# Performance work log

Hardware: AMD Instinct MI355X
Metric: run time of the kernel (lower is better)

The kernel has to match this reference:

```python
import jax, jax.numpy as jnp
import numpy as np

CHUNK = 64

def _l2norm(x, eps=1e-6):
    return x / jnp.sqrt(jnp.sum(x * x, axis=-1, keepdims=True) + eps)

def setup_inputs() -> dict:
    key = jax.random.key(0)
    ks = jax.random.split(key, 5)
    B, S, H, Dk, Dv = 2, 4096, 16, 128, 128
    q = jax.random.normal(ks[0], (B, S, H, Dk), jnp.float32)
    k = jax.random.normal(ks[1], (B, S, H, Dk), jnp.float32)
    v = jax.random.normal(ks[2], (B, S, H, Dv), jnp.float32)
    g = -jax.random.uniform(ks[3], (B, S, H), jnp.float32)          # log-decay, negative
    beta = jax.random.uniform(ks[4], (B, S, H), jnp.float32)        # (0,1) learning rate
    return {"query": q, "key": k, "value": v, "g": g, "beta": beta}

def reference(query, key, value, g, beta):
    C = CHUNK
    init_dtype = query.dtype
    # [b, s, h, d] -> [b, h, s, d], fp32
    q = jnp.transpose(query, (0, 2, 1, 3)).astype(jnp.float32)
    k = jnp.transpose(key, (0, 2, 1, 3)).astype(jnp.float32)
    v = jnp.transpose(value, (0, 2, 1, 3)).astype(jnp.float32)
    gg = jnp.transpose(g, (0, 2, 1)).astype(jnp.float32)
    bb = jnp.transpose(beta, (0, 2, 1)).astype(jnp.float32)
    # use_qk_l2norm_in_kernel=True
    q = _l2norm(q)
    k = _l2norm(k)
    gg = jnp.clip(gg, -20.0, 20.0)
    B, H, S, Dk = k.shape
    Dv = v.shape[-1]
    pad = (-S) % C
    if pad:
        q = jnp.pad(q, ((0, 0), (0, 0), (0, pad), (0, 0)))
        k = jnp.pad(k, ((0, 0), (0, 0), (0, pad), (0, 0)))
        v = jnp.pad(v, ((0, 0), (0, 0), (0, pad), (0, 0)))
        gg = jnp.pad(gg, ((0, 0), (0, 0), (0, pad)))
        bb = jnp.pad(bb, ((0, 0), (0, 0), (0, pad)))
    T = S + pad
    N = T // C
    q = q * (1.0 / np.sqrt(Dk).astype(np.float32))
    v_beta = v * bb[..., None]
    k_beta = k * bb[..., None]
    # chunk: [b, h, n, c, d]
    qc = q.reshape(B, H, N, C, Dk)
    kc = k.reshape(B, H, N, C, Dk)
    vc = v.reshape(B, H, N, C, Dv)
    kbc = k_beta.reshape(B, H, N, C, Dk)
    vbc = v_beta.reshape(B, H, N, C, Dv)
    gc = jnp.cumsum(gg.reshape(B, H, N, C), axis=-1)
    tril = jnp.tril(jnp.ones((C, C), bool))
    strict = jnp.tril(jnp.ones((C, C), bool), -1)
    # decay_mask[i,j] = exp(g_i - g_j) on lower triangle (incl diag), else 0
    gd = gc[..., :, None] - gc[..., None, :]
    decay = jnp.where(tril, jnp.exp(jnp.where(tril, gd, 0.0)), 0.0)
    # UT transform: torch's in-place row loop computes Tm = (I - A)^{-1} with
    # A = -(k_beta @ k^T * decay) on the strictly lower triangle.
    kk = jnp.einsum('bhnik,bhnjk->bhnij', kbc, kc)
    A = jnp.where(strict, -(kk * decay), 0.0)
    I = jnp.eye(C, dtype=jnp.float32)
    Tm = jax.scipy.linalg.solve_triangular(I - A, jnp.broadcast_to(I, A.shape), lower=True, unit_diagonal=True)
    v_ut = jnp.einsum('bhnij,bhnjd->bhnid', Tm, vbc)
    k_cumdecay = jnp.einsum('bhnij,bhnjd->bhnid', Tm, kbc * jnp.exp(gc)[..., None])
    # sequential inter-chunk recurrence
    xs = tuple(jnp.moveaxis(a, 2, 0) for a in (qc, kc, v_ut, k_cumdecay, gc, decay))
    S0 = jnp.zeros((B, H, Dk, Dv), jnp.float32)
    def step(state, x):
        qi, ki, vi, kci, gi, dmi = x
        attn = jnp.where(tril, jnp.einsum('bhik,bhjk->bhij', qi, ki) * dmi, 0.0)
        v_prime = jnp.einsum('bhik,bhkd->bhid', kci, state)
        v_new = vi - v_prime
        inter = jnp.einsum('bhik,bhkd->bhid', qi * jnp.exp(gi)[..., None], state)
        out = inter + jnp.einsum('bhij,bhjd->bhid', attn, v_new)
        g_last = gi[..., -1]
        k_dec = ki * jnp.exp(g_last[..., None] - gi)[..., None]
        new_state = state * jnp.exp(g_last)[..., None, None] + jnp.einsum('bhik,bhid->bhkd', k_dec, v_new)
        return new_state, out
    _, outs = jax.lax.scan(step, S0, xs)  # outs: [n, b, h, c, dv]
    out = jnp.moveaxis(outs, 0, 2).reshape(B, H, T, Dv)[:, :, :S]
    return jnp.transpose(out, (0, 2, 1, 3)).astype(init_dtype)
```

## Files before the change

### kernel.cpp

```cpp
#include <hip/hip_runtime.h>
#include <math.h>


#define CC 64

constexpr int B_  = 2;
constexpr int S_  = 4096;
constexpr int H_  = 16;
constexpr int DK_ = 128;
constexpr int DV_ = 128;
constexpr int NC_  = S_ / CC;
constexpr int NCH_ = B_ * H_ * NC_;
constexpr int W_   = 16;
constexpr int NWB_ = DV_ / W_;

constexpr float QSCALE = 0.08838834764831845f;

constexpr size_t WS_KCUM = 0;
constexpr size_t WS_VUT  = WS_KCUM + (size_t)NCH_ * CC * DK_;
constexpr size_t WS_ATT  = WS_VUT  + (size_t)NCH_ * CC * DV_;
constexpr size_t WS_GC   = WS_ATT  + (size_t)NCH_ * CC * CC;
constexpr size_t WS_END  = WS_GC   + (size_t)NCH_ * CC;

__device__ __forceinline__ float dot4(const float4 a, const float4 b) {
    return a.x * b.x + a.y * b.y + a.z * b.z + a.w * b.w;
}

__global__ __launch_bounds__(256) void gdn_prep(
    const float* __restrict__ q, const float* __restrict__ k,
    const float* __restrict__ v, const float* __restrict__ g,
    const float* __restrict__ beta, float* __restrict__ ws)
{
    const int cid = blockIdx.x;
    const int n   = cid & (NC_ - 1);
    const int bh  = cid / NC_;
    const int h   = bh & (H_ - 1);
    const int b   = bh / H_;
    const int t   = threadIdx.x;
    const int s0  = n * CC;

    __shared__ float s_k[CC][132];
    __shared__ float s_q[CC][132];
    __shared__ float s_u[CC][132];
    __shared__ float s_A[CC][65];
    __shared__ float s_gc[CC];
    __shared__ float s_beta[CC];

    if (t < CC) {
        const size_t gi = ((size_t)b * S_ + s0 + t) * H_ + h;
        float gv = g[gi];
        s_gc[t]   = fminf(fmaxf(gv, -20.f), 20.f);
        s_beta[t] = beta[gi];
    }
    __syncthreads();
    if (t < CC) {
        float x = s_gc[t];
#pragma unroll
        for (int o = 1; o < CC; o <<= 1) {
            float y = __shfl_up(x, o);
            if (t >= o) x += y;
        }
        s_gc[t] = x;
    }

    {
        const int i  = t >> 2;
        const int d0 = (t & 3) * 32;
        const size_t rb = (((size_t)b * S_ + s0 + i) * H_ + h) * (size_t)DK_;
        float4 qr[8], kr[8];
        float ssq = 0.f, ssk = 0.f;
#pragma unroll
        for (int j4 = 0; j4 < 8; ++j4) {
            qr[j4] = *(const float4*)(q + rb + d0 + j4 * 4);
            kr[j4] = *(const float4*)(k + rb + d0 + j4 * 4);
            ssq += dot4(qr[j4], qr[j4]);
            ssk += dot4(kr[j4], kr[j4]);
        }
        ssq += __shfl_xor(ssq, 1); ssq += __shfl_xor(ssq, 2);
        ssk += __shfl_xor(ssk, 1); ssk += __shfl_xor(ssk, 2);
        const float rq = QSCALE / sqrtf(ssq + 1e-6f);
        const float rk = 1.0f   / sqrtf(ssk + 1e-6f);
#pragma unroll
        for (int j4 = 0; j4 < 8; ++j4) {
            *(float4*)&s_q[i][d0 + j4 * 4] =
                make_float4(qr[j4].x * rq, qr[j4].y * rq, qr[j4].z * rq, qr[j4].w * rq);
            *(float4*)&s_k[i][d0 + j4 * 4] =
                make_float4(kr[j4].x * rk, kr[j4].y * rk, kr[j4].z * rk, kr[j4].w * rk);
        }
    }
    __syncthreads();

    {
        const int ti = t >> 4, tj = t & 15;
        const int i0 = ti * 4, j0 = tj * 4;
        float dq[4][4] = {};
        float dkk[4][4] = {};
        if (j0 <= i0 + 3) {
#pragma unroll 2
            for (int d4 = 0; d4 < 32; ++d4) {
                float4 qa[4], ka[4], kb[4];
#pragma unroll
                for (int r = 0; r < 4; ++r) {
                    qa[r] = *(const float4*)&s_q[i0 + r][d4 * 4];
                    ka[r] = *(const float4*)&s_k[i0 + r][d4 * 4];
                    kb[r] = *(const float4*)&s_k[j0 + r][d4 * 4];
                }
#pragma unroll
                for (int r = 0; r < 4; ++r)
#pragma unroll
                    for (int c = 0; c < 4; ++c) {
                        dq[r][c]  += dot4(qa[r], kb[c]);
                        dkk[r][c] += dot4(ka[r], kb[c]);
                    }
            }
        }
        const size_t attb = WS_ATT + (size_t)cid * CC * CC;
#pragma unroll
        for (int r = 0; r < 4; ++r)
#pragma unroll
            for (int c = 0; c < 4; ++c) {
                const int i = i0 + r, j = j0 + c;
                float av = 0.f;
                if (j <= i) {
                    const float dec = expf(s_gc[i] - s_gc[j]);
                    av = dq[r][c] * dec;
                    if (j < i) s_A[i][j] = -(s_beta[i] * dkk[r][c]) * dec;
                }
                ws[attb + i * CC + j] = av;
            }
    }
    __syncthreads();

    {
        const int d = t & 127;
        if (t < 128) {
#pragma unroll 4
            for (int i = 0; i < CC; ++i)
                s_u[i][d] = v[(((size_t)b * S_ + s0 + i) * H_ + h) * (size_t)DV_ + d] * s_beta[i];
        } else {
#pragma unroll 4
            for (int i = 0; i < CC; ++i)
                s_q[i][d] = s_k[i][d] * (s_beta[i] * expf(s_gc[i]));
        }
        float* u = (t < 128) ? &s_u[0][0] : &s_q[0][0];
        for (int blk = 0; blk < 16; ++blk) {
            const int i0 = blk * 4;
            const float u0 = u[(i0 + 0) * 132 + d];
            const float u1 = u[(i0 + 1) * 132 + d] + s_A[i0 + 1][i0] * u0;
            const float u2 = u[(i0 + 2) * 132 + d] + s_A[i0 + 2][i0] * u0 + s_A[i0 + 2][i0 + 1] * u1;
            const float u3 = u[(i0 + 3) * 132 + d] + s_A[i0 + 3][i0] * u0 + s_A[i0 + 3][i0 + 1] * u1
                                                   + s_A[i0 + 3][i0 + 2] * u2;
            u[(i0 + 1) * 132 + d] = u1;
            u[(i0 + 2) * 132 + d] = u2;
            u[(i0 + 3) * 132 + d] = u3;
            for (int i = i0 + 4; i < CC; ++i) {
                const float* Ai = s_A[i];
                u[i * 132 + d] += Ai[i0] * u0 + Ai[i0 + 1] * u1 + Ai[i0 + 2] * u2 + Ai[i0 + 3] * u3;
            }
        }
    }
    __syncthreads();

    {
        const size_t kcb = WS_KCUM + (size_t)cid * CC * DK_;
        const size_t vub = WS_VUT  + (size_t)cid * CC * DV_;
        for (int p = t; p < CC * DK_; p += 256) {
            ws[kcb + p] = s_q[p >> 7][p & 127];
            ws[vub + p] = s_u[p >> 7][p & 127];
        }
        if (t < CC) ws[WS_GC + (size_t)cid * CC + t] = s_gc[t];
    }
}

__global__ __launch_bounds__(256) void gdn_scan(
    const float* __restrict__ q, const float* __restrict__ k,
    const float* __restrict__ ws, float* __restrict__ out)
{
    const int bh  = blockIdx.x & 31;
    const int wb  = blockIdx.x >> 5;
    const int h   = bh & (H_ - 1);
    const int b   = bh / H_;
    const int dv0 = wb * W_;
    const int t   = threadIdx.x;

    __shared__ float s_st[W_][132];
    __shared__ float s_qg[CC][132];
    __shared__ float s_kc[CC][132];
    __shared__ float s_kdT[DK_][CC + 4];
    __shared__ float s_vnT[W_][CC + 4];
    __shared__ float s_at[CC][CC + 4];
    __shared__ float s_gc[CC], s_eg[CC], s_edec[CC];
    __shared__ float s_egl;

    for (int p = t; p < W_ * 132; p += 256) (&s_st[0][0])[p] = 0.f;
    __syncthreads();

    const int dp = t & (W_ - 1);
    const int ig = t >> 4;

    for (int n = 0; n < NC_; ++n) {
        const int cid = bh * NC_ + n;
        const int s0  = n * CC;

        if (t < CC) s_gc[t] = ws[WS_GC + (size_t)cid * CC + t];
        __syncthreads();

        if (t < CC) {
            const float gl = s_gc[CC - 1];
            s_eg[t]   = expf(s_gc[t]);
            s_edec[t] = expf(gl - s_gc[t]);
            if (t == 0) s_egl = expf(gl);
        }
        {
            const size_t kcb = WS_KCUM + (size_t)cid * CC * DK_;
#pragma unroll
            for (int it = 0; it < (CC * DK_) / (256 * 4); ++it) {
                const int p4 = (it * 256 + t) * 4;
                *(float4*)&s_kc[p4 >> 7][p4 & 127] = *(const float4*)(ws + kcb + p4);
            }
            const size_t atb = WS_ATT + (size_t)cid * CC * CC;
#pragma unroll
            for (int it = 0; it < (CC * CC) / (256 * 4); ++it) {
                const int p4 = (it * 256 + t) * 4;
                *(float4*)&s_at[p4 >> 6][p4 & 63] = *(const float4*)(ws + atb + p4);
            }
        }
        __syncthreads();

        {
            const int i  = t >> 2;
            const int d0 = (t & 3) * 32;
            const size_t rb = (((size_t)b * S_ + s0 + i) * H_ + h) * (size_t)DK_;
            float4 qr[8], kr[8];
            float ssq = 0.f, ssk = 0.f;
#pragma unroll
            for (int j4 = 0; j4 < 8; ++j4) {
                qr[j4] = *(const float4*)(q + rb + d0 + j4 * 4);
                kr[j4] = *(const float4*)(k + rb + d0 + j4 * 4);
                ssq += dot4(qr[j4], qr[j4]);
                ssk += dot4(kr[j4], kr[j4]);
            }
            ssq += __shfl_xor(ssq, 1); ssq += __shfl_xor(ssq, 2);
            ssk += __shfl_xor(ssk, 1); ssk += __shfl_xor(ssk, 2);
            const float rq  = QSCALE / sqrtf(ssq + 1e-6f) * s_eg[i];
            const float rkd = s_edec[i] / sqrtf(ssk + 1e-6f);
#pragma unroll
            for (int j4 = 0; j4 < 8; ++j4) {
                *(float4*)&s_qg[i][d0 + j4 * 4] =
                    make_float4(qr[j4].x * rq, qr[j4].y * rq, qr[j4].z * rq, qr[j4].w * rq);
                const int d = d0 + j4 * 4;
                s_kdT[d + 0][i] = kr[j4].x * rkd;
                s_kdT[d + 1][i] = kr[j4].y * rkd;
                s_kdT[d + 2][i] = kr[j4].z * rkd;
                s_kdT[d + 3][i] = kr[j4].w * rkd;
            }
        }
        __syncthreads();

        {
            const size_t vub = WS_VUT + (size_t)cid * CC * DV_ + dv0 + dp;
            float acc[4];
#pragma unroll
            for (int r = 0; r < 4; ++r) acc[r] = ws[vub + (size_t)(ig * 4 + r) * DV_];
            for (int d4 = 0; d4 < 32; ++d4) {
                const float4 st = *(const float4*)&s_st[dp][d4 * 4];
#pragma unroll
                for (int r = 0; r < 4; ++r) {
                    const float4 kc = *(const float4*)&s_kc[ig * 4 + r][d4 * 4];
                    acc[r] -= dot4(kc, st);
                }
            }
#pragma unroll
            for (int r = 0; r < 4; ++r) s_vnT[dp][ig * 4 + r] = acc[r];
        }
        __syncthreads();

        {
            float acc[4] = {0.f, 0.f, 0.f, 0.f};
            for (int d4 = 0; d4 < 32; ++d4) {
                const float4 st = *(const float4*)&s_st[dp][d4 * 4];
#pragma unroll
                for (int r = 0; r < 4; ++r) {
                    const float4 qg = *(const float4*)&s_qg[ig * 4 + r][d4 * 4];
                    acc[r] += dot4(qg, st);
                }
            }
            for (int j4 = 0; j4 < 16; ++j4) {
                const float4 vn = *(const float4*)&s_vnT[dp][j4 * 4];
#pragma unroll
                for (int r = 0; r < 4; ++r) {
                    const float4 at = *(const float4*)&s_at[ig * 4 + r][j4 * 4];
                    acc[r] += dot4(at, vn);
                }
            }
#pragma unroll
            for (int r = 0; r < 4; ++r) {
                const int i = ig * 4 + r;
                out[(((size_t)b * S_ + s0 + i) * H_ + h) * (size_t)DV_ + dv0 + dp] = acc[r];
            }
        }
        __syncthreads();

        {
            const float egl = s_egl;
            float acc[8];
#pragma unroll
            for (int a = 0; a < 8; ++a) acc[a] = s_st[dp][ig + 16 * a] * egl;
            for (int j4 = 0; j4 < 16; ++j4) {
                const float4 vn = *(const float4*)&s_vnT[dp][j4 * 4];
#pragma unroll
                for (int a = 0; a < 8; ++a) {
                    const float4 kd = *(const float4*)&s_kdT[ig + 16 * a][j4 * 4];
                    acc[a] += dot4(kd, vn);
                }
            }
#pragma unroll
            for (int a = 0; a < 8; ++a) s_st[dp][ig + 16 * a] = acc[a];
        }
        __syncthreads();
    }
}

extern "C" void kernel_launch(void* const* d_in, const int* in_sizes, int n_in,
                              void* d_out, int out_size, void* d_ws, size_t ws_size,
                              hipStream_t stream) {
    const float* q    = (const float*)d_in[0];
    const float* k    = (const float*)d_in[1];
    const float* v    = (const float*)d_in[2];
    const float* g    = (const float*)d_in[3];
    const float* beta = (const float*)d_in[4];
    float* ws  = (float*)d_ws;
    float* out = (float*)d_out;

    gdn_prep<<<NCH_, 256, 0, stream>>>(q, k, v, g, beta, ws);
    gdn_scan<<<B_ * H_ * NWB_, 256, 0, stream>>>(q, k, ws, out);
}
```

Baseline: 1.353 ms.

## Rework prep and scan kernels with 512 threads and split-K register tiles

Both kernels move from 256 to 512 threads per block. The matmuls now use 4x4 register tiles with split-K across lanes and shuffle reductions. The scan kernel stores the state as [Dk][Dv] and stacks the k_cumdecay and scaled-q rows into one shared tile, so a single GEMM produces both v_prime and the inter-chunk output. It also fuses the intra-chunk output with the state update behind one barrier, cutting the barriers per chunk. The prep kernel stages the attention matrix in shared memory and writes all workspace tiles with float4 stores. The cost is higher register pressure and extra shuffle traffic.

```diff
diff --git a/kernel.cpp b/kernel.cpp
--- a/kernel.cpp
+++ b/kernel.cpp
@@ -20,13 +20,16 @@
 constexpr size_t WS_VUT  = WS_KCUM + (size_t)NCH_ * CC * DK_;
 constexpr size_t WS_ATT  = WS_VUT  + (size_t)NCH_ * CC * DV_;
 constexpr size_t WS_GC   = WS_ATT  + (size_t)NCH_ * CC * CC;
-constexpr size_t WS_END  = WS_GC   + (size_t)NCH_ * CC;
-
-__device__ __forceinline__ float dot4(const float4 a, const float4 b) {
-    return a.x * b.x + a.y * b.y + a.z * b.z + a.w * b.w;
+
+__device__ __forceinline__ void ld4(float* d, const float* s) {
+    float4 t = *(const float4*)s;
+    d[0] = t.x; d[1] = t.y; d[2] = t.z; d[3] = t.w;
 }
-
-__global__ __launch_bounds__(256) void gdn_prep(
+__device__ __forceinline__ void st4(float* d, const float* s) {
+    *(float4*)d = make_float4(s[0], s[1], s[2], s[3]);
+}
+
+__global__ __launch_bounds__(512) void gdn_prep(
     const float* __restrict__ q, const float* __restrict__ k,
     const float* __restrict__ v, const float* __restrict__ g,
     const float* __restrict__ beta, float* __restrict__ ws)
@@ -41,20 +44,16 @@
 
     __shared__ float s_k[CC][132];
     __shared__ float s_q[CC][132];
-    __shared__ float s_u[CC][132];
-    __shared__ float s_A[CC][65];
+    __shared__ float s_A[CC][66];
+    __shared__ float s_at[CC][68];
     __shared__ float s_gc[CC];
     __shared__ float s_beta[CC];
 
     if (t < CC) {
         const size_t gi = ((size_t)b * S_ + s0 + t) * H_ + h;
         float gv = g[gi];
-        s_gc[t]   = fminf(fmaxf(gv, -20.f), 20.f);
+        float x = fminf(fmaxf(gv, -20.f), 20.f);
         s_beta[t] = beta[gi];
-    }
-    __syncthreads();
-    if (t < CC) {
-        float x = s_gc[t];
 #pragma unroll
         for (int o = 1; o < CC; o <<= 1) {
             float y = __shfl_up(x, o);
@@ -64,61 +63,69 @@
     }
 
     {
-        const int i  = t >> 2;
-        const int d0 = (t & 3) * 32;
+        const int i  = t >> 3;
+        const int d0 = (t & 7) * 16;
         const size_t rb = (((size_t)b * S_ + s0 + i) * H_ + h) * (size_t)DK_;
-        float4 qr[8], kr[8];
+        float qr[4][4], kr[4][4];
         float ssq = 0.f, ssk = 0.f;
 #pragma unroll
-        for (int j4 = 0; j4 < 8; ++j4) {
-            qr[j4] = *(const float4*)(q + rb + d0 + j4 * 4);
-            kr[j4] = *(const float4*)(k + rb + d0 + j4 * 4);
-            ssq += dot4(qr[j4], qr[j4]);
-            ssk += dot4(kr[j4], kr[j4]);
-        }
-        ssq += __shfl_xor(ssq, 1); ssq += __shfl_xor(ssq, 2);
-        ssk += __shfl_xor(ssk, 1); ssk += __shfl_xor(ssk, 2);
+        for (int j4 = 0; j4 < 4; ++j4) {
+            ld4(qr[j4], q + rb + d0 + j4 * 4);
+            ld4(kr[j4], k + rb + d0 + j4 * 4);
+#pragma unroll
+            for (int c = 0; c < 4; ++c) { ssq += qr[j4][c] * qr[j4][c]; ssk += kr[j4][c] * kr[j4][c]; }
+        }
+        ssq += __shfl_xor(ssq, 1); ssq += __shfl_xor(ssq, 2); ssq += __shfl_xor(ssq, 4);
+        ssk += __shfl_xor(ssk, 1); ssk += __shfl_xor(ssk, 2); ssk += __shfl_xor(ssk, 4);
         const float rq = QSCALE / sqrtf(ssq + 1e-6f);
         const float rk = 1.0f   / sqrtf(ssk + 1e-6f);
 #pragma unroll
-        for (int j4 = 0; j4 < 8; ++j4) {
-            *(float4*)&s_q[i][d0 + j4 * 4] =
-                make_float4(qr[j4].x * rq, qr[j4].y * rq, qr[j4].z * rq, qr[j4].w * rq);
-            *(float4*)&s_k[i][d0 + j4 * 4] =
-                make_float4(kr[j4].x * rk, kr[j4].y * rk, kr[j4].z * rk, kr[j4].w * rk);
+        for (int j4 = 0; j4 < 4; ++j4) {
+            float tq[4], tk[4];
+#pragma unroll
+            for (int c = 0; c < 4; ++c) { tq[c] = qr[j4][c] * rq; tk[c] = kr[j4][c] * rk; }
+            st4(&s_q[i][d0 + j4 * 4], tq);
+            st4(&s_k[i][d0 + j4 * 4], tk);
         }
     }
     __syncthreads();
 
     {
-        const int ti = t >> 4, tj = t & 15;
+        const int ks   = t & 1;
+        const int slot = t >> 1;
+        const int tj = (slot & 7) | (((slot >> 5) & 1) << 3);
+        const int ti = ((slot >> 3) & 3) | ((slot >> 6) << 2);
         const int i0 = ti * 4, j0 = tj * 4;
-        float dq[4][4] = {};
-        float dkk[4][4] = {};
+        float dq[4][4] = {}, dkk[4][4] = {};
         if (j0 <= i0 + 3) {
-#pragma unroll 2
-            for (int d4 = 0; d4 < 32; ++d4) {
-                float4 qa[4], ka[4], kb[4];
-#pragma unroll
-                for (int r = 0; r < 4; ++r) {
-                    qa[r] = *(const float4*)&s_q[i0 + r][d4 * 4];
-                    ka[r] = *(const float4*)&s_k[i0 + r][d4 * 4];
-                    kb[r] = *(const float4*)&s_k[j0 + r][d4 * 4];
-                }
+            for (int s = 0; s < 16; ++s) {
+                const int dd = (ks + 2 * s) * 4;
+                float qa[4][4], ka[4][4], kb[4][4];
+#pragma unroll
+                for (int r = 0; r < 4; ++r) { ld4(qa[r], &s_q[i0 + r][dd]); ld4(ka[r], &s_k[i0 + r][dd]); }
+#pragma unroll
+                for (int c = 0; c < 4; ++c) ld4(kb[c], &s_k[j0 + c][dd]);
 #pragma unroll
                 for (int r = 0; r < 4; ++r)
 #pragma unroll
                     for (int c = 0; c < 4; ++c) {
-                        dq[r][c]  += dot4(qa[r], kb[c]);
-                        dkk[r][c] += dot4(ka[r], kb[c]);
+                        dq[r][c]  += qa[r][0]*kb[c][0] + qa[r][1]*kb[c][1] + qa[r][2]*kb[c][2] + qa[r][3]*kb[c][3];
+                        dkk[r][c] += ka[r][0]*kb[c][0] + ka[r][1]*kb[c][1] + ka[r][2]*kb[c][2] + ka[r][3]*kb[c][3];
                     }
             }
         }
-        const size_t attb = WS_ATT + (size_t)cid * CC * CC;
 #pragma unroll
         for (int r = 0; r < 4; ++r)
 #pragma unroll
             for (int c = 0; c < 4; ++c) {
+                float x = dq[r][c];  x += __shfl_xor(x, 1); dq[r][c] = x;
+                float y = dkk[r][c]; y += __shfl_xor(y, 1); dkk[r][c] = y;
+            }
+#pragma unroll
+        for (int r = 0; r < 4; ++r)
+#pragma unroll
+            for (int cc = 0; cc < 2; ++cc) {
+                const int c = ks * 2 + cc;
                 const int i = i0 + r, j = j0 + c;
                 float av = 0.f;
                 if (j <= i) {
@@ -126,23 +133,34 @@
                     av = dq[r][c] * dec;
                     if (j < i) s_A[i][j] = -(s_beta[i] * dkk[r][c]) * dec;
                 }
-                ws[attb + i * CC + j] = av;
+                s_at[i][j] = av;
             }
     }
     __syncthreads();
 
     {
+        const size_t vb = (((size_t)b * S_ + s0) * H_ + h) * (size_t)DV_;
+#pragma unroll
+        for (int r = 0; r < 4; ++r) {
+            const int f4i = r * 512 + t;
+            const int row = f4i >> 5, c4 = (f4i & 31) * 4;
+            float tv[4];
+            ld4(tv, v + vb + (size_t)row * H_ * DV_ + c4);
+            const float be = s_beta[row];
+            tv[0] *= be; tv[1] *= be; tv[2] *= be; tv[3] *= be;
+            st4(&s_q[row][c4], tv);
+            float tk[4];
+            ld4(tk, &s_k[row][c4]);
+            const float sc = be * expf(s_gc[row]);
+            tk[0] *= sc; tk[1] *= sc; tk[2] *= sc; tk[3] *= sc;
+            st4(&s_k[row][c4], tk);
+        }
+    }
+    __syncthreads();
+
+    if (t < 256) {
         const int d = t & 127;
-        if (t < 128) {
-#pragma unroll 4
-            for (int i = 0; i < CC; ++i)
-                s_u[i][d] = v[(((size_t)b * S_ + s0 + i) * H_ + h) * (size_t)DV_ + d] * s_beta[i];
-        } else {
-#pragma unroll 4
-            for (int i = 0; i < CC; ++i)
-                s_q[i][d] = s_k[i][d] * (s_beta[i] * expf(s_gc[i]));
-        }
-        float* u = (t < 128) ? &s_u[0][0] : &s_q[0][0];
+        float* u = (t < 128) ? &s_q[0][0] : &s_k[0][0];
         for (int blk = 0; blk < 16; ++blk) {
             const int i0 = blk * 4;
             const float u0 = u[(i0 + 0) * 132 + d];
@@ -164,15 +182,30 @@
     {
         const size_t kcb = WS_KCUM + (size_t)cid * CC * DK_;
         const size_t vub = WS_VUT  + (size_t)cid * CC * DV_;
-        for (int p = t; p < CC * DK_; p += 256) {
-            ws[kcb + p] = s_q[p >> 7][p & 127];
-            ws[vub + p] = s_u[p >> 7][p & 127];
+#pragma unroll
+        for (int r = 0; r < 4; ++r) {
+            const int f4i = r * 512 + t;
+            const int row = f4i >> 5, c4 = (f4i & 31) * 4;
+            float tk[4], tv[4];
+            ld4(tk, &s_k[row][c4]);
+            ld4(tv, &s_q[row][c4]);
+            st4((float*)(ws + kcb) + f4i * 4, tk);
+            st4((float*)(ws + vub) + f4i * 4, tv);
+        }
+        const size_t atb = WS_ATT + (size_t)cid * CC * CC;
+#pragma unroll
+        for (int r = 0; r < 2; ++r) {
+            const int f4i = r * 512 + t;
+            const int row = f4i >> 4, c4 = (f4i & 15) * 4;
+            float ta[4];
+            ld4(ta, &s_at[row][c4]);
+            st4((float*)(ws + atb) + f4i * 4, ta);
         }
         if (t < CC) ws[WS_GC + (size_t)cid * CC + t] = s_gc[t];
     }
 }
 
-__global__ __launch_bounds__(256) void gdn_scan(
+__global__ __launch_bounds__(512) void gdn_scan(
     const float* __restrict__ q, const float* __restrict__ k,
     const float* __restrict__ ws, float* __restrict__ out)
 {
@@ -183,139 +216,202 @@
     const int dv0 = wb * W_;
     const int t   = threadIdx.x;
 
-    __shared__ float s_st[W_][132];
-    __shared__ float s_qg[CC][132];
-    __shared__ float s_kc[CC][132];
-    __shared__ float s_kdT[DK_][CC + 4];
-    __shared__ float s_vnT[W_][CC + 4];
-    __shared__ float s_at[CC][CC + 4];
-    __shared__ float s_gc[CC], s_eg[CC], s_edec[CC];
-    __shared__ float s_egl;
-
-    for (int p = t; p < W_ * 132; p += 256) (&s_st[0][0])[p] = 0.f;
+    const int ks   = t & 3;
+    const int slot = t >> 2;
+    const int jg   = slot & 3;
+    const int mg   = slot >> 2;
+    const int dp0  = jg * 4;
+
+    __shared__ float s_kq[128][132];
+    __shared__ float s_kd[64][132];
+    __shared__ float s_at[64][68];
+    __shared__ float s_st[128][20];
+    __shared__ float s_vn[64][20];
+    __shared__ float s_o[64][20];
+
+    for (int p = t; p < 128 * 20; p += 512) (&s_st[0][0])[p] = 0.f;
     __syncthreads();
-
-    const int dp = t & (W_ - 1);
-    const int ig = t >> 4;
 
     for (int n = 0; n < NC_; ++n) {
         const int cid = bh * NC_ + n;
         const int s0  = n * CC;
 
-        if (t < CC) s_gc[t] = ws[WS_GC + (size_t)cid * CC + t];
+        const float gl  = ws[WS_GC + (size_t)cid * CC + (CC - 1)];
+        const float egl = expf(gl);
+
+        {
+            const float* kcb = ws + WS_KCUM + (size_t)cid * CC * DK_;
+#pragma unroll
+            for (int r = 0; r < 4; ++r) {
+                const int f4i = r * 512 + t;
+                const int row = f4i >> 5, c4 = (f4i & 31) * 4;
+                float tv[4];
+                ld4(tv, kcb + f4i * 4);
+                st4(&s_kq[row][c4], tv);
+            }
+            const float* atb = ws + WS_ATT + (size_t)cid * CC * CC;
+#pragma unroll
+            for (int r = 0; r < 2; ++r) {
+                const int f4i = r * 512 + t;
+                const int row = f4i >> 4, c4 = (f4i & 15) * 4;
+                float tv[4];
+                ld4(tv, atb + f4i * 4);
+                st4(&s_at[row][c4], tv);
+            }
+        }
+
+        float vut_[4][4];
+        if (ks == 0 && mg < 16) {
+            const float* vub = ws + WS_VUT + (size_t)cid * CC * DV_;
+            const int i0 = mg * 4;
+#pragma unroll
+            for (int r = 0; r < 4; ++r) ld4(vut_[r], vub + (size_t)(i0 + r) * DV_ + dv0 + dp0);
+        }
+
+        {
+            const int i  = t >> 3;
+            const int d0 = (t & 7) * 16;
+            const float gci = ws[WS_GC + (size_t)cid * CC + i];
+            const size_t rb = (((size_t)b * S_ + s0 + i) * H_ + h) * (size_t)DK_;
+            float qr[4][4], kr[4][4];
+            float ssq = 0.f, ssk = 0.f;
+#pragma unroll
+            for (int j4 = 0; j4 < 4; ++j4) {
+                ld4(qr[j4], q + rb + d0 + j4 * 4);
+                ld4(kr[j4], k + rb + d0 + j4 * 4);
+#pragma unroll
+                for (int c = 0; c < 4; ++c) { ssq += qr[j4][c] * qr[j4][c]; ssk += kr[j4][c] * kr[j4][c]; }
+            }
+            ssq += __shfl_xor(ssq, 1); ssq += __shfl_xor(ssq, 2); ssq += __shfl_xor(ssq, 4);
+            ssk += __shfl_xor(ssk, 1); ssk += __shfl_xor(ssk, 2); ssk += __shfl_xor(ssk, 4);
+            const float rq  = QSCALE / sqrtf(ssq + 1e-6f) * expf(gci);
+            const float rkd = expf(gl - gci) / sqrtf(ssk + 1e-6f);
+#pragma unroll
+            for (int j4 = 0; j4 < 4; ++j4) {
+                float tq[4], tk[4];
+#pragma unroll
+                for (int c = 0; c < 4; ++c) { tq[c] = qr[j4][c] * rq; tk[c] = kr[j4][c] * rkd; }
+                st4(&s_kq[64 + i][d0 + j4 * 4], tq);
+                st4(&s_kd[i][d0 + j4 * 4], tk);
+            }
+        }
         __syncthreads();
 
-        if (t < CC) {
-            const float gl = s_gc[CC - 1];
-            s_eg[t]   = expf(s_gc[t]);
-            s_edec[t] = expf(gl - s_gc[t]);
-            if (t == 0) s_egl = expf(gl);
-        }
         {
-            const size_t kcb = WS_KCUM + (size_t)cid * CC * DK_;
-#pragma unroll
-            for (int it = 0; it < (CC * DK_) / (256 * 4); ++it) {
-                const int p4 = (it * 256 + t) * 4;
-                *(float4*)&s_kc[p4 >> 7][p4 & 127] = *(const float4*)(ws + kcb + p4);
-            }
-            const size_t atb = WS_ATT + (size_t)cid * CC * CC;
-#pragma unroll
-            for (int it = 0; it < (CC * CC) / (256 * 4); ++it) {
-                const int p4 = (it * 256 + t) * 4;
-                *(float4*)&s_at[p4 >> 6][p4 & 63] = *(const float4*)(ws + atb + p4);
+            const int m0 = mg * 4;
+            float acc[4][4] = {};
+            for (int s = 0; s < 8; ++s) {
+                const int dk = (ks + 4 * s) * 4;
+                float Bv[4][4], Av[4][4];
+#pragma unroll
+                for (int kk = 0; kk < 4; ++kk) ld4(Bv[kk], &s_st[dk + kk][dp0]);
+#pragma unroll
+                for (int r = 0; r < 4; ++r) ld4(Av[r], &s_kq[m0 + r][dk]);
+#pragma unroll
+                for (int r = 0; r < 4; ++r)
+#pragma unroll
+                    for (int c = 0; c < 4; ++c)
+                        acc[r][c] += Av[r][0]*Bv[0][c] + Av[r][1]*Bv[1][c]
+                                   + Av[r][2]*Bv[2][c] + Av[r][3]*Bv[3][c];
+            }
+#pragma unroll
+            for (int r = 0; r < 4; ++r)
+#pragma unroll
+                for (int c = 0; c < 4; ++c) {
+                    float x = acc[r][c];
+                    x += __shfl_xor(x, 1); x += __shfl_xor(x, 2);
+                    acc[r][c] = x;
+                }
+            if (ks == 0) {
+                if (mg < 16) {
+                    const int i0 = mg * 4;
+#pragma unroll
+                    for (int r = 0; r < 4; ++r) {
+                        float tv[4];
+#pragma unroll
+                        for (int c = 0; c < 4; ++c) tv[c] = vut_[r][c] - acc[r][c];
+                        st4(&s_vn[i0 + r][dp0], tv);
+                    }
+                } else {
+                    const int i0 = (mg - 16) * 4;
+#pragma unroll
+                    for (int r = 0; r < 4; ++r) st4(&s_o[i0 + r][dp0], acc[r]);
+                }
             }
         }
         __syncthreads();
 
         {
-            const int i  = t >> 2;
-            const int d0 = (t & 3) * 32;
-            const size_t rb = (((size_t)b * S_ + s0 + i) * H_ + h) * (size_t)DK_;
-            float4 qr[8], kr[8];
-            float ssq = 0.f, ssk = 0.f;
-#pragma unroll
-            for (int j4 = 0; j4 < 8; ++j4) {
-                qr[j4] = *(const float4*)(q + rb + d0 + j4 * 4);
-                kr[j4] = *(const float4*)(k + rb + d0 + j4 * 4);
-                ssq += dot4(qr[j4], qr[j4]);
-                ssk += dot4(kr[j4], kr[j4]);
-            }
-            ssq += __shfl_xor(ssq, 1); ssq += __shfl_xor(ssq, 2);
-            ssk += __shfl_xor(ssk, 1); ssk += __shfl_xor(ssk, 2);
-            const float rq  = QSCALE / sqrtf(ssq + 1e-6f) * s_eg[i];
-            const float rkd = s_edec[i] / sqrtf(ssk + 1e-6f);
-#pragma unroll
-            for (int j4 = 0; j4 < 8; ++j4) {
-                *(float4*)&s_qg[i][d0 + j4 * 4] =
-                    make_float4(qr[j4].x * rq, qr[j4].y * rq, qr[j4].z * rq, qr[j4].w * rq);
-                const int d = d0 + j4 * 4;
-                s_kdT[d + 0][i] = kr[j4].x * rkd;
-                s_kdT[d + 1][i] = kr[j4].y * rkd;
-                s_kdT[d + 2][i] = kr[j4].z * rkd;
-                s_kdT[d + 3][i] = kr[j4].w * rkd;
-            }
-        }
-        __syncthreads();
-
+            const int i0b = mg * 2;
+            float bacc[2][4] = {};
+            for (int s = 0; s < 4; ++s) {
+                const int j = (ks + 4 * s) * 4;
+                float vnv[4][4], atv[2][4];
+#pragma unroll
+                for (int kk = 0; kk < 4; ++kk) ld4(vnv[kk], &s_vn[j + kk][dp0]);
+#pragma unroll
+                for (int r = 0; r < 2; ++r) ld4(atv[r], &s_at[i0b + r][j]);
+#pragma unroll
+                for (int r = 0; r < 2; ++r)
+#pragma unroll
+                    for (int c = 0; c < 4; ++c)
+                        bacc[r][c] += atv[r][0]*vnv[0][c] + atv[r][1]*vnv[1][c]
+                                    + atv[r][2]*vnv[2][c] + atv[r][3]*vnv[3][c];
+            }
+#pragma unroll
+            for (int r = 0; r < 2; ++r)
+#pragma unroll
+                for (int c = 0; c < 4; ++c) {
+                    float x = bacc[r][c];
+                    x += __shfl_xor(x, 1); x += __shfl_xor(x, 2);
+                    bacc[r][c] = x;
+                }
+            if (ks == 0) {
+#pragma unroll
+                for (int r = 0; r < 2; ++r) {
+                    float ov[4];
+                    ld4(ov, &s_o[i0b + r][dp0]);
+#pragma unroll
+                    for (int c = 0; c < 4; ++c) ov[c] += bacc[r][c];
+                    st4(out + (((size_t)b * S_ + s0 + i0b + r) * H_ + h) * (size_t)DV_ + dv0 + dp0, ov);
+                }
+            }
+        }
         {
-            const size_t vub = WS_VUT + (size_t)cid * CC * DV_ + dv0 + dp;
-            float acc[4];
-#pragma unroll
-            for (int r = 0; r < 4; ++r) acc[r] = ws[vub + (size_t)(ig * 4 + r) * DV_];
-            for (int d4 = 0; d4 < 32; ++d4) {
-                const float4 st = *(const float4*)&s_st[dp][d4 * 4];
+            const int dk0 = mg * 4;
+            float cacc[4][4] = {};
+            for (int s = 0; s < 4; ++s) {
+                const int ib = (ks + 4 * s) * 4;
+#pragma unroll
+                for (int kk = 0; kk < 4; ++kk) {
+                    float kdv[4], vnv[4];
+                    ld4(kdv, &s_kd[ib + kk][dk0]);
+                    ld4(vnv, &s_vn[ib + kk][dp0]);
+#pragma unroll
+                    for (int r = 0; r < 4; ++r)
+#pragma unroll
+                        for (int c = 0; c < 4; ++c)
+                            cacc[r][c] += kdv[r] * vnv[c];
+                }
+            }
+#pragma unroll
+            for (int r = 0; r < 4; ++r)
+#pragma unroll
+                for (int c = 0; c < 4; ++c) {
+                    float x = cacc[r][c];
+                    x += __shfl_xor(x, 1); x += __shfl_xor(x, 2);
+                    cacc[r][c] = x;
+                }
+            if (ks == 0) {
 #pragma unroll
                 for (int r = 0; r < 4; ++r) {
-                    const float4 kc = *(const float4*)&s_kc[ig * 4 + r][d4 * 4];
-                    acc[r] -= dot4(kc, st);
-                }
-            }
-#pragma unroll
-            for (int r = 0; r < 4; ++r) s_vnT[dp][ig * 4 + r] = acc[r];
-        }
-        __syncthreads();
-
-        {
-            float acc[4] = {0.f, 0.f, 0.f, 0.f};
-            for (int d4 = 0; d4 < 32; ++d4) {
-                const float4 st = *(const float4*)&s_st[dp][d4 * 4];
-#pragma unroll
-                for (int r = 0; r < 4; ++r) {
-                    const float4 qg = *(const float4*)&s_qg[ig * 4 + r][d4 * 4];
-                    acc[r] += dot4(qg, st);
-                }
-            }
-            for (int j4 = 0; j4 < 16; ++j4) {
-                const float4 vn = *(const float4*)&s_vnT[dp][j4 * 4];
-#pragma unroll
-                for (int r = 0; r < 4; ++r) {
-                    const float4 at = *(const float4*)&s_at[ig * 4 + r][j4 * 4];
-                    acc[r] += dot4(at, vn);
-                }
-            }
-#pragma unroll
-            for (int r = 0; r < 4; ++r) {
-                const int i = ig * 4 + r;
-                out[(((size_t)b * S_ + s0 + i) * H_ + h) * (size_t)DV_ + dv0 + dp] = acc[r];
-            }
-        }
-        __syncthreads();
-
-        {
-            const float egl = s_egl;
-            float acc[8];
-#pragma unroll
-            for (int a = 0; a < 8; ++a) acc[a] = s_st[dp][ig + 16 * a] * egl;
-            for (int j4 = 0; j4 < 16; ++j4) {
-                const float4 vn = *(const float4*)&s_vnT[dp][j4 * 4];
-#pragma unroll
-                for (int a = 0; a < 8; ++a) {
-                    const float4 kd = *(const float4*)&s_kdT[ig + 16 * a][j4 * 4];
-                    acc[a] += dot4(kd, vn);
-                }
-            }
-#pragma unroll
-            for (int a = 0; a < 8; ++a) s_st[dp][ig + 16 * a] = acc[a];
+                    float st_[4];
+                    ld4(st_, &s_st[dk0 + r][dp0]);
+#pragma unroll
+                    for (int c = 0; c < 4; ++c) st_[c] = st_[c] * egl + cacc[r][c];
+                    st4(&s_st[dk0 + r][dp0], st_);
+                }
+            }
         }
         __syncthreads();
     }
@@ -332,6 +428,6 @@
     float* ws  = (float*)d_ws;
     float* out = (float*)d_out;
 
-    gdn_prep<<<NCH_, 256, 0, stream>>>(q, k, v, g, beta, ws);
-    gdn_scan<<<B_ * H_ * NWB_, 256, 0, stream>>>(q, k, ws, out);
+    gdn_prep<<<NCH_, 512, 0, stream>>>(q, k, v, g, beta, ws);
+    gdn_scan<<<B_ * H_ * NWB_, 512, 0, stream>>>(q, k, ws, out);
 }
```

Result: faster. 1.086 ms (-19.7%).
